# Performance work log

Hardware: AMD Instinct MI355X
Metric: run time of the kernel (lower is better)

Reference implementation:

```python
import jax, jax.numpy as jnp
import numpy as np

B, GRID, DM, DEPTH = 4, 12, 384, 8
L = GRID ** 3                      # 1728 tokens
DI, NS, DC, DTR = 768, 16, 4, 24   # d_inner, d_state, d_conv, dt_rank
KEEP = 432


def _sincos_pos_embed(grid, dim):
    g = np.arange(grid, dtype=np.float32)
    gh, gw, gd = np.meshgrid(g, g, g, indexing='ij')
    pd = dim // 6
    omega = 1.0 / (10000.0 ** (np.arange(pd, dtype=np.float32) / pd))
    parts = []
    for v in (gh, gw, gd):
        o = np.einsum('m,d->md', v.reshape(-1), omega)
        parts += [np.sin(o), np.cos(o)]
    return np.concatenate(parts, axis=1)[None].astype(np.float32)  # (1, L, dim)


def setup_inputs():
    key = jax.random.key(0)
    ks = jax.random.split(key, 16)
    n = lambda k, s, sc=0.02: jax.random.normal(k, s, jnp.float32) * sc
    # mamba dt_proj bias init: inverse softplus of dt ~ LogUniform(1e-3, 1e-1)
    dt = jnp.exp(jax.random.uniform(ks[9], (DEPTH, DI)) * (np.log(0.1) - np.log(0.001)) + np.log(0.001))
    dt_proj_b = dt + jnp.log(-jnp.expm1(-dt))
    A_log = jnp.log(jnp.broadcast_to(jnp.arange(1, NS + 1, dtype=jnp.float32), (DEPTH, DI, NS)))
    rng = np.random.default_rng(0)
    act = np.zeros((B, L), np.int32)
    for b in range(B):
        act[b, rng.permutation(L)[:KEEP]] = 1
    return {
        'imgs': n(ks[0], (B, DM, GRID, GRID, GRID), 1.0),
        'pos_embed': jnp.asarray(_sincos_pos_embed(GRID, DM)),
        'mask_token': n(ks[1], (DM,)),
        'norm1_w': jnp.ones((DEPTH, DM)), 'norm1_b': jnp.zeros((DEPTH, DM)),
        'in_proj_w': n(ks[2], (DEPTH, 2 * DI, DM)),
        'conv_w': n(ks[3], (DEPTH, DI, DC), 0.1), 'conv_b': jnp.zeros((DEPTH, DI)),
        'x_proj_w': n(ks[4], (DEPTH, DTR + 2 * NS, DI)),
        'dt_proj_w': n(ks[5], (DEPTH, DI, DTR), 0.1), 'dt_proj_b': dt_proj_b,
        'A_log': A_log, 'A_b_log': A_log,
        'D_skip': jnp.ones((DEPTH, DI)),
        'out_proj_w': n(ks[6], (DEPTH, DM, DI)),
        'norm2_w': jnp.ones((DEPTH, DM)), 'norm2_b': jnp.zeros((DEPTH, DM)),
        'fc1_w': n(ks[7], (DEPTH, 2 * DM, DM)), 'fc1_b': jnp.zeros((DEPTH, 2 * DM)),
        'fc2_w': n(ks[8], (DEPTH, DM, 2 * DM)), 'fc2_b': jnp.zeros((DEPTH, DM)),
        'active': jnp.asarray(act.reshape(B, 1, GRID, GRID, GRID)),
        'len_keep': KEEP,
    }


def _ln(x, w, b):
    mu = jnp.mean(x, -1, keepdims=True)
    v = jnp.var(x, -1, keepdims=True)
    return (x - mu) * jax.lax.rsqrt(v + 1e-5) * w + b


def _ssm_dir(xr, z, conv_w, conv_b, xpw, dtw, dtb, a_log, dskip):
    # xr, z: (B, DI, Lk) pre-conv streams; causal depthwise conv then selective scan
    Lk = xr.shape[-1]
    xp = jnp.pad(xr, ((0, 0), (0, 0), (DC - 1, 0)))
    x = sum(conv_w[:, k][None, :, None] * xp[:, :, k:k + Lk] for k in range(DC))
    x = jax.nn.silu(x + conv_b[None, :, None])
    xdb = jnp.einsum('bdl,rd->brl', x, xpw)
    dtr, Bm, Cm = xdb[:, :DTR], xdb[:, DTR:DTR + NS], xdb[:, DTR + NS:]
    delta = jax.nn.softplus(jnp.einsum('brl,dr->bdl', dtr, dtw) + dtb[None, :, None])
    A = -jnp.exp(a_log)                              # (DI, NS)
    dl = delta.transpose(0, 2, 1)                    # (B, Lk, DI)
    xt = x.transpose(0, 2, 1)                        # (B, Lk, DI)
    dA = jnp.exp(dl[..., None] * A)                  # (B, Lk, DI, NS)
    dBx = dl[..., None] * Bm.transpose(0, 2, 1)[:, :, None, :] * xt[..., None]
    Ct = Cm.transpose(0, 2, 1)                       # (B, Lk, NS)

    def step(h, inp):
        a, bx, c = inp
        h = a * h + bx
        return h, jnp.einsum('bdn,bn->bd', h, c)

    h0 = jnp.zeros((xr.shape[0], DI, NS), xr.dtype)
    _, ys = jax.lax.scan(step, h0, (dA.transpose(1, 0, 2, 3), dBx.transpose(1, 0, 2, 3), Ct.transpose(1, 0, 2)))
    y = ys.transpose(1, 0, 2) + dskip * xt           # (B, Lk, DI)
    return y * jax.nn.silu(z.transpose(0, 2, 1))


def _block(x, p):
    (n1w, n1b, inW, cw, cb, xpw, dtw, dtb, al, abl, dsk, ow, n2w, n2b, f1w, f1b, f2w, f2b) = p
    h = _ln(x, n1w, n1b)
    xz = h @ inW.T                                   # (B, Lk, 2*DI)
    xr = xz[..., :DI].transpose(0, 2, 1)
    z = xz[..., DI:].transpose(0, 2, 1)
    yf = _ssm_dir(xr, z, cw, cb, xpw, dtw, dtb, al, dsk)
    yb = _ssm_dir(xr[:, :, ::-1], z[:, :, ::-1], cw, cb, xpw, dtw, dtb, abl, dsk)[:, ::-1]
    x = x + (yf + yb) @ ow.T
    h2 = _ln(x, n2w, n2b)
    return x + (jax.nn.gelu(h2 @ f1w.T + f1b, approximate=False) @ f2w.T + f2b)


def _forward(imgs, pos_embed, mask_token, norm1_w, norm1_b, in_proj_w, conv_w, conv_b,
             x_proj_w, dt_proj_w, dt_proj_b, A_log, A_b_log, D_skip, out_proj_w,
             norm2_w, norm2_b, fc1_w, fc1_b, fc2_w, fc2_b, active, len_keep):
    x = imgs.reshape(B, DM, L).transpose(0, 2, 1) + pos_embed   # (B, L, DM)
    mask = active.reshape(B, L).astype(jnp.int32)               # (B, L) 1=keep
    ids_shuffle = jnp.argsort(1 - mask, axis=1)                 # kept tokens first
    ids_restore = jnp.argsort(ids_shuffle, axis=1)
    ids_keep = ids_shuffle[:, :len_keep]
    xk = jnp.take_along_axis(x, jnp.broadcast_to(ids_keep[:, :, None], (B, len_keep, DM)), axis=1)
    blk = jax.checkpoint(_block)
    for i in range(DEPTH):
        p = (norm1_w[i], norm1_b[i], in_proj_w[i], conv_w[i], conv_b[i], x_proj_w[i],
             dt_proj_w[i], dt_proj_b[i], A_log[i], A_b_log[i], D_skip[i], out_proj_w[i],
             norm2_w[i], norm2_b[i], fc1_w[i], fc1_b[i], fc2_w[i], fc2_b[i])
        xk = blk(xk, p)
    mt = jnp.broadcast_to(mask_token, (B, L - len_keep, DM))
    x_ = jnp.concatenate([xk, mt], axis=1)
    x = jnp.take_along_axis(x_, jnp.broadcast_to(ids_restore[:, :, None], (B, L, DM)), axis=1)
    return x.transpose(0, 2, 1).reshape(B, DM, GRID, GRID, GRID)


def reference(imgs, pos_embed, mask_token, norm1_w, norm1_b, in_proj_w, conv_w, conv_b,
              x_proj_w, dt_proj_w, dt_proj_b, A_log, A_b_log, D_skip, out_proj_w,
              norm2_w, norm2_b, fc1_w, fc1_b, fc2_w, fc2_b, active, len_keep):
    return _forward(imgs, pos_embed, mask_token, norm1_w, norm1_b, in_proj_w, conv_w, conv_b,
                    x_proj_w, dt_proj_w, dt_proj_b, A_log, A_b_log, D_skip, out_proj_w,
                    norm2_w, norm2_b, fc1_w, fc1_b, fc2_w, fc2_b, active, len_keep)
```

## Files before the change

### kernel.cpp

```cpp
#include <hip/hip_runtime.h>
#include <hip/hip_bf16.h>
#include <math.h>

#define B_    4
#define GRID_ 12
#define DM_   384
#define DEPTH_ 8
#define L_    1728
#define DI_   768
#define NS_   16
#define DC_   4
#define DTR_  24
#define KEEP_ 432
#define XPR_  56
#define NC_   16
#define CL_   27
#define XSPLIT_ 4

typedef __attribute__((ext_vector_type(8))) short short8;
typedef __attribute__((ext_vector_type(4))) float floatx4;

__device__ __forceinline__ float silu_f(float x) {
    return x / (1.0f + __expf(-x));
}
__device__ __forceinline__ float softplus_f(float x) {
    return (x > 20.0f) ? x : log1pf(expf(x));
}
__device__ __forceinline__ float gelu_exact_f(float x) {
    return 0.5f * x * (1.0f + erff(x * 0.7071067811865476f));
}
__device__ __forceinline__ unsigned short f2bf(float x) {
    union { float f; unsigned int u; } c; c.f = x;
    unsigned int u = c.u;
    unsigned int r = (u + 0x7fffu + ((u >> 16) & 1u)) >> 16;
    return (unsigned short)r;
}

#define S0_ (DEPTH_ * 2 * DI_ * DM_)
#define S1_ (DEPTH_ * XPR_ * DI_)
#define S3_ (DEPTH_ * DM_ * DI_)
#define S4_ (DEPTH_ * 2 * DM_ * DM_)
#define S5_ (DEPTH_ * DM_ * 2 * DM_)
#define WTOT_ (S0_ + S1_ + S3_ + S4_ + S5_)

__global__ void cast_weights_k(const float* __restrict__ w0,
                               const float* __restrict__ w1,
                               const float* __restrict__ w3,
                               const float* __restrict__ w4,
                               const float* __restrict__ w5,
                               unsigned short* __restrict__ out) {
    int i = blockIdx.x * 256 + threadIdx.x;
    if (i >= WTOT_) return;
    float v;
    if (i < S0_) v = w0[i];
    else if (i < S0_ + S1_) v = w1[i - S0_];
    else if (i < S0_ + S1_ + S3_) v = w3[i - S0_ - S1_];
    else if (i < S0_ + S1_ + S3_ + S4_) v = w4[i - S0_ - S1_ - S3_];
    else v = w5[i - S0_ - S1_ - S3_ - S4_];
    out[i] = f2bf(v);
}

__global__ __launch_bounds__(256) void compute_ids_k(
        const int* __restrict__ active,
        int* __restrict__ RANK, int* __restrict__ IDS) {
    __shared__ int cnt[256];
    int b = blockIdx.x;
    int t = threadIdx.x;
    const int PER = (L_ + 255) / 256;
    int base = t * PER;
    int c = 0;
    for (int j = 0; j < PER; ++j) {
        int l = base + j;
        if (l < L_ && active[b * L_ + l]) ++c;
    }
    cnt[t] = c;
    __syncthreads();
    for (int off = 1; off < 256; off <<= 1) {
        int v = (t >= off) ? cnt[t - off] : 0;
        __syncthreads();
        cnt[t] += v;
        __syncthreads();
    }
    int r = cnt[t] - c;
    for (int j = 0; j < PER; ++j) {
        int l = base + j;
        if (l >= L_) break;
        if (active[b * L_ + l]) {
            RANK[b * L_ + l] = r;
            IDS[b * KEEP_ + r] = l;
            ++r;
        } else {
            RANK[b * L_ + l] = -1;
        }
    }
}

__global__ void gather_embed_k(const float* __restrict__ imgs,
                               const float* __restrict__ pos,
                               const int* __restrict__ IDS,
                               float* __restrict__ X) {
    int tid = blockIdx.x * 256 + threadIdx.x;
    if (tid >= B_ * KEEP_ * DM_) return;
    int c = tid % DM_;
    int i = (tid / DM_) % KEEP_;
    int b = tid / (DM_ * KEEP_);
    int l = IDS[b * KEEP_ + i];
    X[tid] = imgs[((size_t)b * DM_ + c) * L_ + l] + pos[(size_t)l * DM_ + c];
}

__global__ void final_scatter_k(const float* __restrict__ X,
                                const float* __restrict__ mask_token,
                                const int* __restrict__ RANK,
                                float* __restrict__ out) {
    int tid = blockIdx.x * 256 + threadIdx.x;
    if (tid >= B_ * DM_ * L_) return;
    int l = tid % L_;
    int c = (tid / L_) % DM_;
    int b = tid / (L_ * DM_);
    int r = RANK[b * L_ + l];
    out[tid] = (r >= 0) ? X[((size_t)b * KEEP_ + r) * DM_ + c] : mask_token[c];
}

__global__ void layernorm_k(const float* __restrict__ X,
                            const float* __restrict__ w,
                            const float* __restrict__ bia,
                            unsigned short* __restrict__ H, int rows) {
    int row = blockIdx.x * 4 + (threadIdx.x >> 6);
    int lane = threadIdx.x & 63;
    if (row >= rows) return;
    const float* x = X + (size_t)row * DM_;
    float v[6];
    float s = 0.0f;
#pragma unroll
    for (int j = 0; j < 6; ++j) { v[j] = x[lane + 64 * j]; s += v[j]; }
#pragma unroll
    for (int m = 1; m < 64; m <<= 1) s += __shfl_xor(s, m);
    float mu = s * (1.0f / DM_);
    float s2 = 0.0f;
#pragma unroll
    for (int j = 0; j < 6; ++j) { float d = v[j] - mu; s2 += d * d; }
#pragma unroll
    for (int m = 1; m < 64; m <<= 1) s2 += __shfl_xor(s2, m);
    float rs = rsqrtf(s2 * (1.0f / DM_) + 1e-5f);
    unsigned short* h = H + (size_t)row * DM_;
#pragma unroll
    for (int j = 0; j < 6; ++j) {
        int c = lane + 64 * j;
        h[c] = f2bf((v[j] - mu) * rs * w[c] + bia[c]);
    }
}

#define APAD_ 40
__global__ __launch_bounds__(256) void gemm_mfma_k(
    const void* __restrict__ Ap, const float* __restrict__ A2, int lda,
    int abf16,
    const unsigned short* __restrict__ Wb,
    const float* __restrict__ bias,
    float* __restrict__ C, int ldc,
    int M, int N, int K, int kslices, int mode) {
    __shared__ unsigned short As[2][64][APAD_];
    __shared__ unsigned short Bs[2][64][APAD_];
    int t = threadIdx.x;
    int wave = t >> 6;
    int lane = t & 63;
    int q = lane >> 4;
    int ml = lane & 15;
    int m0 = blockIdx.y * 64;
    int n0 = blockIdx.x * 64;
    int z  = blockIdx.z;
    int Kper = K / kslices;
    int kbeg = z * Kper;

    int srow = t >> 2;
    int scol = (t & 3) * 8;

    floatx4 acc[4];
#pragma unroll
    for (int i = 0; i < 4; ++i) acc[i] = (floatx4){0.f, 0.f, 0.f, 0.f};

    float ra[8];
    uint4 rau, rb;

    auto loadA = [&](int k0) {
        if (abf16) {
            rau = *(const uint4*)((const unsigned short*)Ap +
                                  (size_t)(m0 + srow) * lda + k0 + scol);
        } else {
            const float* ap = (const float*)Ap + (size_t)(m0 + srow) * lda + k0 + scol;
            floatx4 v0 = *(const floatx4*)ap;
            floatx4 v1 = *(const floatx4*)(ap + 4);
            if (A2) {
                const float* ap2 = A2 + (size_t)(m0 + srow) * lda + k0 + scol;
                v0 += *(const floatx4*)ap2;
                v1 += *(const floatx4*)(ap2 + 4);
            }
#pragma unroll
            for (int j = 0; j < 4; ++j) { ra[j] = v0[j]; ra[4 + j] = v1[j]; }
        }
    };
    auto loadB = [&](int k0) {
        rb = *(const uint4*)(Wb + (size_t)(n0 + srow) * K + k0 + scol);
    };
    auto storeT = [&](int buf) {
        if (abf16) {
            *(uint4*)&As[buf][srow][scol] = rau;
        } else {
#pragma unroll
            for (int j = 0; j < 8; ++j) As[buf][srow][scol + j] = f2bf(ra[j]);
        }
        *(uint4*)&Bs[buf][srow][scol] = rb;
    };

    int nk = Kper >> 5;
    loadA(kbeg);
    loadB(kbeg);
    storeT(0);
    __syncthreads();
    int buf = 0;
    for (int it = 0; it < nk; ++it) {
        if (it + 1 < nk) {
            int kn = kbeg + (it + 1) * 32;
            loadA(kn);
            loadB(kn);
        }
        short8 a = *(const short8*)&As[buf][wave * 16 + ml][q * 8];
#pragma unroll
        for (int ns = 0; ns < 4; ++ns) {
            short8 b = *(const short8*)&Bs[buf][ns * 16 + ml][q * 8];
            acc[ns] = __builtin_amdgcn_mfma_f32_16x16x32_bf16(a, b, acc[ns], 0, 0, 0);
        }
        if (it + 1 < nk) {
            storeT(buf ^ 1);
            __syncthreads();
            buf ^= 1;
        }
    }

#pragma unroll
    for (int ns = 0; ns < 4; ++ns) {
        int n = n0 + ns * 16 + ml;
#pragma unroll
        for (int r = 0; r < 4; ++r) {
            int m = m0 + wave * 16 + q * 4 + r;
            float v = acc[ns][r];
            size_t ci = (size_t)m * ldc + n;
            if (mode == 6) {
                atomicAdd(&C[ci], v);
            } else if (mode == 7) {
                if (z == 0) v += bias[n];
                atomicAdd(&C[ci], v);
            } else if (mode == 9) {
                ((unsigned short*)C)[ci] = f2bf(gelu_exact_f(v + bias[n]));
            } else {
                C[ci] = v;
            }
        }
    }
}

__global__ __launch_bounds__(256) void xproj_conv_k(
        const float* __restrict__ XZ,
        const float* __restrict__ cw,
        const float* __restrict__ cb,
        const unsigned short* __restrict__ Wb,
        float* __restrict__ Cout) {
    __shared__ unsigned short As[2][64][APAD_];
    __shared__ unsigned short Bs[2][64][APAD_];
    int t = threadIdx.x;
    int wave = t >> 6;
    int lane = t & 63;
    int q = lane >> 4;
    int ml = lane & 15;
    int m0 = blockIdx.y * 64;
    int z  = blockIdx.z;
    const int Kper = DI_ / XSPLIT_;
    int kbeg = z * Kper;
    float* C = Cout + (size_t)z * (2 * B_ * KEEP_) * XPR_;

    int srow = t >> 2;
    int scol = (t & 3) * 8;
    int m = m0 + srow;
    int dir = m / (B_ * KEEP_);
    int rem = m - dir * (B_ * KEEP_);
    int b = rem / KEEP_;
    int s = rem - b * KEEP_;

    floatx4 acc[4];
#pragma unroll
    for (int i = 0; i < 4; ++i) acc[i] = (floatx4){0.f, 0.f, 0.f, 0.f};

    float ra[8];
    uint4 rb;

    auto loadA = [&](int k0) {
        int d0 = k0 + scol;
        float v[8];
        {
            floatx4 c0v = *(const floatx4*)(cb + d0);
            floatx4 c1v = *(const floatx4*)(cb + d0 + 4);
#pragma unroll
            for (int j = 0; j < 4; ++j) { v[j] = c0v[j]; v[4 + j] = c1v[j]; }
        }
        float cwv[8][4];
#pragma unroll
        for (int jj = 0; jj < 8; ++jj) {
            floatx4 cv = *(const floatx4*)(cw + (size_t)(d0 + jj) * 4);
#pragma unroll
            for (int j = 0; j < 4; ++j) cwv[jj][j] = cv[j];
        }
#pragma unroll
        for (int j = 0; j < DC_; ++j) {
            int pos = s - (DC_ - 1) + j;
            if (pos >= 0) {
                int la = dir ? (KEEP_ - 1 - pos) : pos;
                const float* xp = XZ + ((size_t)b * KEEP_ + la) * (2 * DI_) + d0;
                floatx4 x0 = *(const floatx4*)xp;
                floatx4 x1 = *(const floatx4*)(xp + 4);
#pragma unroll
                for (int jj = 0; jj < 4; ++jj) v[jj] += cwv[jj][j] * x0[jj];
#pragma unroll
                for (int jj = 0; jj < 4; ++jj) v[4 + jj] += cwv[4 + jj][j] * x1[jj];
            }
        }
#pragma unroll
        for (int jj = 0; jj < 8; ++jj) ra[jj] = silu_f(v[jj]);
    };
    auto loadB = [&](int k0) {
        if (srow < XPR_) {
            rb = *(const uint4*)(Wb + (size_t)srow * DI_ + k0 + scol);
        } else {
            rb = (uint4){0u, 0u, 0u, 0u};
        }
    };
    auto storeT = [&](int buf) {
#pragma unroll
        for (int j = 0; j < 8; ++j) As[buf][srow][scol + j] = f2bf(ra[j]);
        *(uint4*)&Bs[buf][srow][scol] = rb;
    };

    const int nk = Kper >> 5;
    loadA(kbeg);
    loadB(kbeg);
    storeT(0);
    __syncthreads();
    int buf = 0;
    for (int it = 0; it < nk; ++it) {
        if (it + 1 < nk) {
            int kn = kbeg + (it + 1) * 32;
            loadA(kn);
            loadB(kn);
        }
        short8 a = *(const short8*)&As[buf][wave * 16 + ml][q * 8];
#pragma unroll
        for (int ns = 0; ns < 4; ++ns) {
            short8 b2 = *(const short8*)&Bs[buf][ns * 16 + ml][q * 8];
            acc[ns] = __builtin_amdgcn_mfma_f32_16x16x32_bf16(a, b2, acc[ns], 0, 0, 0);
        }
        if (it + 1 < nk) {
            storeT(buf ^ 1);
            __syncthreads();
            buf ^= 1;
        }
    }
#pragma unroll
    for (int ns = 0; ns < 4; ++ns) {
        int n = ns * 16 + ml;
        if (n >= XPR_) continue;
#pragma unroll
        for (int r = 0; r < 4; ++r) {
            int mm = m0 + wave * 16 + q * 4 + r;
            C[(size_t)mm * XPR_ + n] = acc[ns][r];
        }
    }
}

#define PSL_ ((size_t)(2 * B_ * KEEP_) * XPR_)

__global__ __launch_bounds__(256) void scan_partial_k(
        const float* __restrict__ XZ,
        const float* __restrict__ PART,
        const float* __restrict__ cw,
        const float* __restrict__ cb,
        const float* __restrict__ dtw,
        const float* __restrict__ dtb,
        const float* __restrict__ Alog,
        const float* __restrict__ Ablog,
        float* __restrict__ HFIN,
        float* __restrict__ SDELT) {
    __shared__ float sXR[CL_ + 3][256];
    __shared__ float sXDB[CL_][XPR_];
    int blk = blockIdx.x;
    int g   = blk % 3;
    int c   = (blk / 3) % NC_;
    int b   = (blk / (3 * NC_)) % B_;
    int dir = blk / (3 * NC_ * B_);
    int t = threadIdx.x;
    int d = g * 256 + t;
    int c0 = c * CL_;

    for (int r = 0; r < CL_ + 3; ++r) {
        int pos = c0 - 3 + r;
        float v = 0.0f;
        if (pos >= 0) {
            int la = dir ? (KEEP_ - 1 - pos) : pos;
            v = XZ[((size_t)b * KEEP_ + la) * (2 * DI_) + d];
        }
        sXR[r][t] = v;
    }
    size_t rbase = ((size_t)(dir * B_ + b) * KEEP_ + c0) * XPR_;
    for (int i = t; i < CL_ * XPR_; i += 256) {
        size_t idx = rbase + i;
        float v = PART[idx];
#pragma unroll
        for (int sl = 1; sl < XSPLIT_; ++sl) v += PART[idx + sl * PSL_];
        sXDB[i / XPR_][i % XPR_] = v;
    }
    __syncthreads();

    float cwv[DC_];
    {
        floatx4 cv = *(const floatx4*)(cw + (size_t)d * 4);
#pragma unroll
        for (int j = 0; j < DC_; ++j) cwv[j] = cv[j];
    }
    float cbv = cb[d];
    float dtwv[DTR_];
#pragma unroll
    for (int r = 0; r < DTR_ / 4; ++r) {
        floatx4 v = *(const floatx4*)(dtw + (size_t)d * DTR_ + r * 4);
#pragma unroll
        for (int j = 0; j < 4; ++j) dtwv[r * 4 + j] = v[j];
    }
    float dtbv = dtb[d];
    const float* alog = dir ? Ablog : Alog;
    float Av[NS_];
#pragma unroll
    for (int n = 0; n < NS_; ++n) Av[n] = -__expf(alog[(size_t)d * NS_ + n]);

    float h[NS_];
#pragma unroll
    for (int n = 0; n < NS_; ++n) h[n] = 0.0f;
    float sdel = 0.0f;

    for (int s = 0; s < CL_; ++s) {
        float xv = cbv;
#pragma unroll
        for (int j = 0; j < DC_; ++j) xv += cwv[j] * sXR[s + j][t];
        xv = silu_f(xv);
        float dt = dtbv;
#pragma unroll
        for (int r = 0; r < DTR_; ++r) dt += dtwv[r] * sXDB[s][r];
        dt = softplus_f(dt);
        sdel += dt;
        float dx = dt * xv;
#pragma unroll
        for (int n = 0; n < NS_; ++n)
            h[n] = __expf(dt * Av[n]) * h[n] + dx * sXDB[s][DTR_ + n];
    }
    size_t o = ((size_t)(dir * B_ + b) * NC_ + c) * DI_ + d;
    SDELT[o] = sdel;
#pragma unroll
    for (int n = 0; n < NS_; ++n) HFIN[o * NS_ + n] = h[n];
}

__global__ __launch_bounds__(256) void scan_combine_k(
        const float* __restrict__ HFIN,
        const float* __restrict__ SDELT,
        const float* __restrict__ Alog,
        const float* __restrict__ Ablog,
        float* __restrict__ HINIT) {
    int gid = blockIdx.x * 256 + threadIdx.x;
    int n = gid & 15;
    int d = (gid >> 4) % DI_;
    int b = (gid / (16 * DI_)) % B_;
    int dir = gid / (16 * DI_ * B_);
    const float* alog = dir ? Ablog : Alog;
    float Av = -__expf(alog[(size_t)d * NS_ + n]);
    float hi = 0.0f;
#pragma unroll
    for (int c = 0; c < NC_; ++c) {
        size_t o = ((size_t)(dir * B_ + b) * NC_ + c) * DI_ + d;
        HINIT[o * NS_ + n] = hi;
        hi = __expf(Av * SDELT[o]) * hi + HFIN[o * NS_ + n];
    }
}

__global__ __launch_bounds__(256) void scan_final_k(
        const float* __restrict__ XZ,
        const float* __restrict__ PART,
        const float* __restrict__ cw,
        const float* __restrict__ cb,
        const float* __restrict__ dtw,
        const float* __restrict__ dtb,
        const float* __restrict__ Alog,
        const float* __restrict__ Ablog,
        const float* __restrict__ dskip,
        const float* __restrict__ HINIT,
        float* __restrict__ YOUT) {
    __shared__ float sXR[CL_ + 3][256];
    __shared__ float sZ[CL_][256];
    __shared__ float sXDB[CL_][XPR_];
    int blk = blockIdx.x;
    int g   = blk % 3;
    int c   = (blk / 3) % NC_;
    int b   = (blk / (3 * NC_)) % B_;
    int dir = blk / (3 * NC_ * B_);
    int t = threadIdx.x;
    int d = g * 256 + t;
    int c0 = c * CL_;

    for (int r = 0; r < CL_ + 3; ++r) {
        int pos = c0 - 3 + r;
        float v = 0.0f;
        if (pos >= 0) {
            int la = dir ? (KEEP_ - 1 - pos) : pos;
            v = XZ[((size_t)b * KEEP_ + la) * (2 * DI_) + d];
        }
        sXR[r][t] = v;
    }
    for (int s = 0; s < CL_; ++s) {
        int pos = c0 + s;
        int la = dir ? (KEEP_ - 1 - pos) : pos;
        sZ[s][t] = XZ[((size_t)b * KEEP_ + la) * (2 * DI_) + DI_ + d];
    }
    size_t rbase = ((size_t)(dir * B_ + b) * KEEP_ + c0) * XPR_;
    for (int i = t; i < CL_ * XPR_; i += 256) {
        size_t idx = rbase + i;
        float v = PART[idx];
#pragma unroll
        for (int sl = 1; sl < XSPLIT_; ++sl) v += PART[idx + sl * PSL_];
        sXDB[i / XPR_][i % XPR_] = v;
    }
    __syncthreads();

    float cwv[DC_];
    {
        floatx4 cv = *(const floatx4*)(cw + (size_t)d * 4);
#pragma unroll
        for (int j = 0; j < DC_; ++j) cwv[j] = cv[j];
    }
    float cbv = cb[d];
    float dtwv[DTR_];
#pragma unroll
    for (int r = 0; r < DTR_ / 4; ++r) {
        floatx4 v = *(const floatx4*)(dtw + (size_t)d * DTR_ + r * 4);
#pragma unroll
        for (int j = 0; j < 4; ++j) dtwv[r * 4 + j] = v[j];
    }
    float dtbv = dtb[d];
    const float* alog = dir ? Ablog : Alog;
    float Av[NS_];
#pragma unroll
    for (int n = 0; n < NS_; ++n) Av[n] = -__expf(alog[(size_t)d * NS_ + n]);
    float dsk = dskip[d];

    size_t o = ((size_t)(dir * B_ + b) * NC_ + c) * DI_ + d;
    float h[NS_];
#pragma unroll
    for (int n = 0; n < NS_; ++n) h[n] = HINIT[o * NS_ + n];

    for (int s = 0; s < CL_; ++s) {
        float xv = cbv;
#pragma unroll
        for (int j = 0; j < DC_; ++j) xv += cwv[j] * sXR[s + j][t];
        xv = silu_f(xv);
        float dt = dtbv;
#pragma unroll
        for (int r = 0; r < DTR_; ++r) dt += dtwv[r] * sXDB[s][r];
        dt = softplus_f(dt);
        float dx = dt * xv;
        float y = 0.0f;
#pragma unroll
        for (int n = 0; n < NS_; ++n) {
            h[n] = __expf(dt * Av[n]) * h[n] + dx * sXDB[s][DTR_ + n];
            y += h[n] * sXDB[s][DTR_ + NS_ + n];
        }
        int pos = c0 + s;
        int la = dir ? (KEEP_ - 1 - pos) : pos;
        YOUT[((size_t)(dir * B_ + b) * KEEP_ + la) * DI_ + d] =
            (y + dsk * xv) * silu_f(sZ[s][t]);
    }
}

extern "C" void kernel_launch(void* const* d_in, const int* in_sizes, int n_in,
                              void* d_out, int out_size, void* d_ws, size_t ws_size,
                              hipStream_t stream) {
    const float* imgs      = (const float*)d_in[0];
    const float* pos       = (const float*)d_in[1];
    const float* mask_tok  = (const float*)d_in[2];
    const float* n1w       = (const float*)d_in[3];
    const float* n1b       = (const float*)d_in[4];
    const float* inW       = (const float*)d_in[5];
    const float* cw        = (const float*)d_in[6];
    const float* cb        = (const float*)d_in[7];
    const float* xpw       = (const float*)d_in[8];
    const float* dtw       = (const float*)d_in[9];
    const float* dtb       = (const float*)d_in[10];
    const float* Alog      = (const float*)d_in[11];
    const float* Ablog     = (const float*)d_in[12];
    const float* dskip     = (const float*)d_in[13];
    const float* ow        = (const float*)d_in[14];
    const float* n2w       = (const float*)d_in[15];
    const float* n2b       = (const float*)d_in[16];
    const float* f1w       = (const float*)d_in[17];
    const float* f1b       = (const float*)d_in[18];
    const float* f2w       = (const float*)d_in[19];
    const float* f2b       = (const float*)d_in[20];
    const int*   active    = (const int*)d_in[21];
    float* out = (float*)d_out;

    char* w = (char*)d_ws;
    auto alloc = [&](size_t bytes) {
        void* p = (void*)w;
        w += (bytes + 255) & ~(size_t)255;
        return p;
    };
    int*   RANK  = (int*)  alloc((size_t)B_ * L_ * 4);
    int*   IDS   = (int*)  alloc((size_t)B_ * KEEP_ * 4);
    float* X     = (float*)alloc((size_t)B_ * KEEP_ * DM_ * 4);
    unsigned short* Hb = (unsigned short*)alloc((size_t)B_ * KEEP_ * DM_ * 2);
    float* XZ    = (float*)alloc((size_t)B_ * KEEP_ * 2 * DI_ * 4);
    float* PART  = (float*)alloc((size_t)XSPLIT_ * 2 * B_ * KEEP_ * XPR_ * 4);
    float* YOUT  = (float*)alloc((size_t)2 * B_ * KEEP_ * DI_ * 4);
    unsigned short* Gb = (unsigned short*)alloc((size_t)B_ * KEEP_ * DI_ * 2);
    float* HFIN  = (float*)alloc((size_t)2 * B_ * NC_ * DI_ * NS_ * 4);
    float* HINIT = (float*)alloc((size_t)2 * B_ * NC_ * DI_ * NS_ * 4);
    float* SDELT = (float*)alloc((size_t)2 * B_ * NC_ * DI_ * 4);
    unsigned short* WB = (unsigned short*)alloc((size_t)WTOT_ * 2);

    const unsigned short* wInB = WB;
    const unsigned short* wXpB = WB + S0_;
    const unsigned short* wOwB = WB + S0_ + S1_;
    const unsigned short* wF1B = WB + S0_ + S1_ + S3_;
    const unsigned short* wF2B = WB + S0_ + S1_ + S3_ + S4_;

    const int ROWS = B_ * KEEP_;
    const int ROWS2 = 2 * B_ * KEEP_;
    const int SCAN_BLOCKS = 2 * B_ * NC_ * 3;

    cast_weights_k<<<(WTOT_ + 255) / 256, 256, 0, stream>>>(
        inW, xpw, ow, f1w, f2w, (unsigned short*)WB);
    compute_ids_k<<<B_, 256, 0, stream>>>(active, RANK, IDS);
    gather_embed_k<<<(B_ * KEEP_ * DM_ + 255) / 256, 256, 0, stream>>>(imgs, pos, IDS, X);

    for (int layer = 0; layer < DEPTH_; ++layer) {
        const unsigned short* L_inW = wInB + (size_t)layer * 2 * DI_ * DM_;
        const float* L_cw  = cw  + (size_t)layer * DI_ * DC_;
        const float* L_cb  = cb  + (size_t)layer * DI_;
        const unsigned short* L_xpw = wXpB + (size_t)layer * XPR_ * DI_;
        const float* L_dtw = dtw + (size_t)layer * DI_ * DTR_;
        const float* L_dtb = dtb + (size_t)layer * DI_;
        const float* L_Al  = Alog  + (size_t)layer * DI_ * NS_;
        const float* L_Abl = Ablog + (size_t)layer * DI_ * NS_;
        const float* L_dsk = dskip + (size_t)layer * DI_;
        const unsigned short* L_ow  = wOwB + (size_t)layer * DM_ * DI_;
        const unsigned short* L_f1w = wF1B + (size_t)layer * 2 * DM_ * DM_;
        const float* L_f1b = f1b + (size_t)layer * 2 * DM_;
        const unsigned short* L_f2w = wF2B + (size_t)layer * DM_ * 2 * DM_;
        const float* L_f2b = f2b + (size_t)layer * DM_;

        layernorm_k<<<(ROWS + 3) / 4, 256, 0, stream>>>(
            X, n1w + layer * DM_, n1b + layer * DM_, Hb, ROWS);
        gemm_mfma_k<<<dim3((2 * DI_) / 64, ROWS / 64), 256, 0, stream>>>(
            Hb, nullptr, DM_, 1, L_inW, nullptr, XZ, 2 * DI_,
            ROWS, 2 * DI_, DM_, 1, 0);
        xproj_conv_k<<<dim3(1, ROWS2 / 64, XSPLIT_), 256, 0, stream>>>(
            XZ, L_cw, L_cb, L_xpw, PART);
        scan_partial_k<<<SCAN_BLOCKS, 256, 0, stream>>>(
            XZ, PART, L_cw, L_cb, L_dtw, L_dtb, L_Al, L_Abl, HFIN, SDELT);
        scan_combine_k<<<(2 * B_ * DI_ * NS_) / 256, 256, 0, stream>>>(
            HFIN, SDELT, L_Al, L_Abl, HINIT);
        scan_final_k<<<SCAN_BLOCKS, 256, 0, stream>>>(
            XZ, PART, L_cw, L_cb, L_dtw, L_dtb, L_Al, L_Abl, L_dsk, HINIT, YOUT);
        gemm_mfma_k<<<dim3(DM_ / 64, ROWS / 64, 2), 256, 0, stream>>>(
            YOUT, YOUT + (size_t)B_ * KEEP_ * DI_, DI_, 0, L_ow, nullptr,
            X, DM_, ROWS, DM_, DI_, 2, 6);
        layernorm_k<<<(ROWS + 3) / 4, 256, 0, stream>>>(
            X, n2w + layer * DM_, n2b + layer * DM_, Hb, ROWS);
        gemm_mfma_k<<<dim3((2 * DM_) / 64, ROWS / 64), 256, 0, stream>>>(
            Hb, nullptr, DM_, 1, L_f1w, L_f1b, (float*)Gb, 2 * DM_,
            ROWS, 2 * DM_, DM_, 1, 9);
        gemm_mfma_k<<<dim3(DM_ / 64, ROWS / 64, 2), 256, 0, stream>>>(
            Gb, nullptr, 2 * DM_, 1, L_f2w, L_f2b, X, DM_,
            ROWS, DM_, 2 * DM_, 2, 7);
    }

    final_scatter_k<<<(B_ * DM_ * L_ + 255) / 256, 256, 0, stream>>>(
        X, mask_tok, RANK, out);
}
```

Before: 1.488 ms.

## Exploit geometric A structure in scan, shorten chunks, drop shared staging

Scan kernels check at runtime whether A_n equals (n+1)*A_0 and, if so, compute the per-state decays as successive powers of one exponential instead of 16 exps. Chunk length drops from 27 to 9 (48 chunks) to raise parallelism, conv inputs are streamed through registers instead of shared memory, and softplus uses fast intrinsics. The chunk-state buffers are merged into one d-contiguous array updated in place by the combine kernel. It risks a longer serial combine and slight precision differences from the power chaining.

```diff
diff --git a/kernel.cpp b/kernel.cpp
--- a/kernel.cpp
+++ b/kernel.cpp
@@ -13,8 +13,8 @@
 #define DTR_  24
 #define KEEP_ 432
 #define XPR_  56
-#define NC_   16
-#define CL_   27
+#define NC_   48
+#define CL_   9
 #define XSPLIT_ 4
 
 typedef __attribute__((ext_vector_type(8))) short short8;
@@ -24,7 +24,7 @@
     return x / (1.0f + __expf(-x));
 }
 __device__ __forceinline__ float softplus_f(float x) {
-    return (x > 20.0f) ? x : log1pf(expf(x));
+    return (x > 20.0f) ? x : __logf(1.0f + __expf(x));
 }
 __device__ __forceinline__ float gelu_exact_f(float x) {
     return 0.5f * x * (1.0f + erff(x * 0.7071067811865476f));
@@ -376,6 +376,18 @@
 
 #define PSL_ ((size_t)(2 * B_ * KEEP_) * XPR_)
 
+__device__ __forceinline__ bool a_geometric(const float* alog, int d, float& Av0) {
+    Av0 = -__expf(alog[(size_t)d * NS_]);
+    bool fast = true;
+#pragma unroll
+    for (int n = 1; n < NS_; ++n) {
+        float av = -__expf(alog[(size_t)d * NS_ + n]);
+        float ref = (float)(n + 1) * Av0;
+        fast = fast && (fabsf(av - ref) <= 1e-4f * fabsf(ref));
+    }
+    return fast;
+}
+
 __global__ __launch_bounds__(256) void scan_partial_k(
         const float* __restrict__ XZ,
         const float* __restrict__ PART,
@@ -385,9 +397,8 @@
         const float* __restrict__ dtb,
         const float* __restrict__ Alog,
         const float* __restrict__ Ablog,
-        float* __restrict__ HFIN,
+        float* __restrict__ HS,
         float* __restrict__ SDELT) {
-    __shared__ float sXR[CL_ + 3][256];
     __shared__ float sXDB[CL_][XPR_];
     int blk = blockIdx.x;
     int g   = blk % 3;
@@ -397,17 +408,9 @@
     int t = threadIdx.x;
     int d = g * 256 + t;
     int c0 = c * CL_;
-
-    for (int r = 0; r < CL_ + 3; ++r) {
-        int pos = c0 - 3 + r;
-        float v = 0.0f;
-        if (pos >= 0) {
-            int la = dir ? (KEEP_ - 1 - pos) : pos;
-            v = XZ[((size_t)b * KEEP_ + la) * (2 * DI_) + d];
-        }
-        sXR[r][t] = v;
-    }
-    size_t rbase = ((size_t)(dir * B_ + b) * KEEP_ + c0) * XPR_;
+    int dirb = dir * B_ + b;
+
+    size_t rbase = ((size_t)dirb * KEEP_ + c0) * XPR_;
     for (int i = t; i < CL_ * XPR_; i += 256) {
         size_t idx = rbase + i;
         float v = PART[idx];
@@ -417,12 +420,7 @@
     }
     __syncthreads();
 
-    float cwv[DC_];
-    {
-        floatx4 cv = *(const floatx4*)(cw + (size_t)d * 4);
-#pragma unroll
-        for (int j = 0; j < DC_; ++j) cwv[j] = cv[j];
-    }
+    floatx4 cwv = *(const floatx4*)(cw + (size_t)d * 4);
     float cbv = cb[d];
     float dtwv[DTR_];
 #pragma unroll
@@ -433,55 +431,89 @@
     }
     float dtbv = dtb[d];
     const float* alog = dir ? Ablog : Alog;
-    float Av[NS_];
-#pragma unroll
-    for (int n = 0; n < NS_; ++n) Av[n] = -__expf(alog[(size_t)d * NS_ + n]);
+    float Av0;
+    bool fast = a_geometric(alog, d, Av0);
+
+    auto xr_at = [&](int pos) -> float {
+        if (pos < 0) return 0.0f;
+        int la = dir ? (KEEP_ - 1 - pos) : pos;
+        return XZ[((size_t)b * KEEP_ + la) * (2 * DI_) + d];
+    };
+    float w0 = xr_at(c0 - 3), w1 = xr_at(c0 - 2), w2 = xr_at(c0 - 1);
 
     float h[NS_];
 #pragma unroll
     for (int n = 0; n < NS_; ++n) h[n] = 0.0f;
     float sdel = 0.0f;
 
-    for (int s = 0; s < CL_; ++s) {
-        float xv = cbv;
-#pragma unroll
-        for (int j = 0; j < DC_; ++j) xv += cwv[j] * sXR[s + j][t];
-        xv = silu_f(xv);
-        float dt = dtbv;
-#pragma unroll
-        for (int r = 0; r < DTR_; ++r) dt += dtwv[r] * sXDB[s][r];
-        dt = softplus_f(dt);
-        sdel += dt;
-        float dx = dt * xv;
-#pragma unroll
-        for (int n = 0; n < NS_; ++n)
-            h[n] = __expf(dt * Av[n]) * h[n] + dx * sXDB[s][DTR_ + n];
-    }
-    size_t o = ((size_t)(dir * B_ + b) * NC_ + c) * DI_ + d;
-    SDELT[o] = sdel;
-#pragma unroll
-    for (int n = 0; n < NS_; ++n) HFIN[o * NS_ + n] = h[n];
+    if (fast) {
+#pragma unroll
+        for (int s = 0; s < CL_; ++s) {
+            float w3 = xr_at(c0 + s);
+            float xv = silu_f(cbv + cwv[0] * w0 + cwv[1] * w1 + cwv[2] * w2 + cwv[3] * w3);
+            w0 = w1; w1 = w2; w2 = w3;
+            float dt = dtbv;
+#pragma unroll
+            for (int r = 0; r < DTR_; ++r) dt += dtwv[r] * sXDB[s][r];
+            dt = softplus_f(dt);
+            sdel += dt;
+            float dx = dt * xv;
+            float e1 = __expf(dt * Av0);
+            float e = e1;
+#pragma unroll
+            for (int n = 0; n < NS_; ++n) {
+                h[n] = e * h[n] + dx * sXDB[s][DTR_ + n];
+                e *= e1;
+            }
+        }
+    } else {
+        for (int s = 0; s < CL_; ++s) {
+            float w3 = xr_at(c0 + s);
+            float xv = silu_f(cbv + cwv[0] * w0 + cwv[1] * w1 + cwv[2] * w2 + cwv[3] * w3);
+            w0 = w1; w1 = w2; w2 = w3;
+            float dt = dtbv;
+            for (int r = 0; r < DTR_; ++r) dt += dtwv[r] * sXDB[s][r];
+            dt = softplus_f(dt);
+            sdel += dt;
+            float dx = dt * xv;
+            for (int n = 0; n < NS_; ++n) {
+                float av = -__expf(alog[(size_t)d * NS_ + n]);
+                h[n] = __expf(dt * av) * h[n] + dx * sXDB[s][DTR_ + n];
+            }
+        }
+    }
+    size_t ob = ((size_t)dirb * NC_ + c) * NS_;
+    SDELT[((size_t)dirb * NC_ + c) * DI_ + d] = sdel;
+#pragma unroll
+    for (int n = 0; n < NS_; ++n) HS[(ob + n) * DI_ + d] = h[n];
 }
 
 __global__ __launch_bounds__(256) void scan_combine_k(
-        const float* __restrict__ HFIN,
+        float* __restrict__ HS,
         const float* __restrict__ SDELT,
         const float* __restrict__ Alog,
-        const float* __restrict__ Ablog,
-        float* __restrict__ HINIT) {
+        const float* __restrict__ Ablog) {
     int gid = blockIdx.x * 256 + threadIdx.x;
-    int n = gid & 15;
-    int d = (gid >> 4) % DI_;
-    int b = (gid / (16 * DI_)) % B_;
-    int dir = gid / (16 * DI_ * B_);
+    int d = gid % DI_;
+    int n = (gid / DI_) % NS_;
+    int b = (gid / (DI_ * NS_)) % B_;
+    int dir = gid / (DI_ * NS_ * B_);
+    int dirb = dir * B_ + b;
     const float* alog = dir ? Ablog : Alog;
     float Av = -__expf(alog[(size_t)d * NS_ + n]);
     float hi = 0.0f;
-#pragma unroll
+    size_t sbase = (size_t)dirb * NC_ * DI_ + d;
+    size_t hbase = ((size_t)dirb * NC_ * NS_ + n) * DI_ + d;
+    float sd_n = SDELT[sbase];
+    float hf_n = HS[hbase];
     for (int c = 0; c < NC_; ++c) {
-        size_t o = ((size_t)(dir * B_ + b) * NC_ + c) * DI_ + d;
-        HINIT[o * NS_ + n] = hi;
-        hi = __expf(Av * SDELT[o]) * hi + HFIN[o * NS_ + n];
+        float sd = sd_n, hf = hf_n;
+        if (c + 1 < NC_) {
+            sd_n = SDELT[sbase + (size_t)(c + 1) * DI_];
+            hf_n = HS[hbase + (size_t)(c + 1) * NS_ * DI_];
+        }
+        HS[hbase + (size_t)c * NS_ * DI_] = hi;
+        hi = __expf(Av * sd) * hi + hf;
     }
 }
 
@@ -495,10 +527,8 @@
         const float* __restrict__ Alog,
         const float* __restrict__ Ablog,
         const float* __restrict__ dskip,
-        const float* __restrict__ HINIT,
+        const float* __restrict__ HS,
         float* __restrict__ YOUT) {
-    __shared__ float sXR[CL_ + 3][256];
-    __shared__ float sZ[CL_][256];
     __shared__ float sXDB[CL_][XPR_];
     int blk = blockIdx.x;
     int g   = blk % 3;
@@ -508,22 +538,9 @@
     int t = threadIdx.x;
     int d = g * 256 + t;
     int c0 = c * CL_;
-
-    for (int r = 0; r < CL_ + 3; ++r) {
-        int pos = c0 - 3 + r;
-        float v = 0.0f;
-        if (pos >= 0) {
-            int la = dir ? (KEEP_ - 1 - pos) : pos;
-            v = XZ[((size_t)b * KEEP_ + la) * (2 * DI_) + d];
-        }
-        sXR[r][t] = v;
-    }
-    for (int s = 0; s < CL_; ++s) {
-        int pos = c0 + s;
-        int la = dir ? (KEEP_ - 1 - pos) : pos;
-        sZ[s][t] = XZ[((size_t)b * KEEP_ + la) * (2 * DI_) + DI_ + d];
-    }
-    size_t rbase = ((size_t)(dir * B_ + b) * KEEP_ + c0) * XPR_;
+    int dirb = dir * B_ + b;
+
+    size_t rbase = ((size_t)dirb * KEEP_ + c0) * XPR_;
     for (int i = t; i < CL_ * XPR_; i += 256) {
         size_t idx = rbase + i;
         float v = PART[idx];
@@ -533,12 +550,7 @@
     }
     __syncthreads();
 
-    float cwv[DC_];
-    {
-        floatx4 cv = *(const floatx4*)(cw + (size_t)d * 4);
-#pragma unroll
-        for (int j = 0; j < DC_; ++j) cwv[j] = cv[j];
-    }
+    floatx4 cwv = *(const floatx4*)(cw + (size_t)d * 4);
     float cbv = cb[d];
     float dtwv[DTR_];
 #pragma unroll
@@ -549,36 +561,69 @@
     }
     float dtbv = dtb[d];
     const float* alog = dir ? Ablog : Alog;
-    float Av[NS_];
-#pragma unroll
-    for (int n = 0; n < NS_; ++n) Av[n] = -__expf(alog[(size_t)d * NS_ + n]);
+    float Av0;
+    bool fast = a_geometric(alog, d, Av0);
     float dsk = dskip[d];
 
-    size_t o = ((size_t)(dir * B_ + b) * NC_ + c) * DI_ + d;
     float h[NS_];
-#pragma unroll
-    for (int n = 0; n < NS_; ++n) h[n] = HINIT[o * NS_ + n];
-
-    for (int s = 0; s < CL_; ++s) {
-        float xv = cbv;
-#pragma unroll
-        for (int j = 0; j < DC_; ++j) xv += cwv[j] * sXR[s + j][t];
-        xv = silu_f(xv);
-        float dt = dtbv;
-#pragma unroll
-        for (int r = 0; r < DTR_; ++r) dt += dtwv[r] * sXDB[s][r];
-        dt = softplus_f(dt);
-        float dx = dt * xv;
-        float y = 0.0f;
-#pragma unroll
-        for (int n = 0; n < NS_; ++n) {
-            h[n] = __expf(dt * Av[n]) * h[n] + dx * sXDB[s][DTR_ + n];
-            y += h[n] * sXDB[s][DTR_ + NS_ + n];
-        }
-        int pos = c0 + s;
+    size_t hbase = ((size_t)dirb * NC_ + c) * NS_;
+#pragma unroll
+    for (int n = 0; n < NS_; ++n) h[n] = HS[(hbase + n) * DI_ + d];
+
+    auto xr_at = [&](int pos) -> float {
+        if (pos < 0) return 0.0f;
         int la = dir ? (KEEP_ - 1 - pos) : pos;
-        YOUT[((size_t)(dir * B_ + b) * KEEP_ + la) * DI_ + d] =
-            (y + dsk * xv) * silu_f(sZ[s][t]);
+        return XZ[((size_t)b * KEEP_ + la) * (2 * DI_) + d];
+    };
+    float w0 = xr_at(c0 - 3), w1 = xr_at(c0 - 2), w2 = xr_at(c0 - 1);
+
+    if (fast) {
+#pragma unroll
+        for (int s = 0; s < CL_; ++s) {
+            int pos = c0 + s;
+            int la = dir ? (KEEP_ - 1 - pos) : pos;
+            float w3 = XZ[((size_t)b * KEEP_ + la) * (2 * DI_) + d];
+            float zg = XZ[((size_t)b * KEEP_ + la) * (2 * DI_) + DI_ + d];
+            float xv = silu_f(cbv + cwv[0] * w0 + cwv[1] * w1 + cwv[2] * w2 + cwv[3] * w3);
+            w0 = w1; w1 = w2; w2 = w3;
+            float dt = dtbv;
+#pragma unroll
+            for (int r = 0; r < DTR_; ++r) dt += dtwv[r] * sXDB[s][r];
+            dt = softplus_f(dt);
+            float dx = dt * xv;
+            float e1 = __expf(dt * Av0);
+            float e = e1;
+            float y = 0.0f;
+#pragma unroll
+            for (int n = 0; n < NS_; ++n) {
+                h[n] = e * h[n] + dx * sXDB[s][DTR_ + n];
+                y += h[n] * sXDB[s][DTR_ + NS_ + n];
+                e *= e1;
+            }
+            YOUT[((size_t)dirb * KEEP_ + la) * DI_ + d] =
+                (y + dsk * xv) * silu_f(zg);
+        }
+    } else {
+        for (int s = 0; s < CL_; ++s) {
+            int pos = c0 + s;
+            int la = dir ? (KEEP_ - 1 - pos) : pos;
+            float w3 = XZ[((size_t)b * KEEP_ + la) * (2 * DI_) + d];
+            float zg = XZ[((size_t)b * KEEP_ + la) * (2 * DI_) + DI_ + d];
+            float xv = silu_f(cbv + cwv[0] * w0 + cwv[1] * w1 + cwv[2] * w2 + cwv[3] * w3);
+            w0 = w1; w1 = w2; w2 = w3;
+            float dt = dtbv;
+            for (int r = 0; r < DTR_; ++r) dt += dtwv[r] * sXDB[s][r];
+            dt = softplus_f(dt);
+            float dx = dt * xv;
+            float y = 0.0f;
+            for (int n = 0; n < NS_; ++n) {
+                float av = -__expf(alog[(size_t)d * NS_ + n]);
+                h[n] = __expf(dt * av) * h[n] + dx * sXDB[s][DTR_ + n];
+                y += h[n] * sXDB[s][DTR_ + NS_ + n];
+            }
+            YOUT[((size_t)dirb * KEEP_ + la) * DI_ + d] =
+                (y + dsk * xv) * silu_f(zg);
+        }
     }
 }
 
@@ -623,8 +668,7 @@
     float* PART  = (float*)alloc((size_t)XSPLIT_ * 2 * B_ * KEEP_ * XPR_ * 4);
     float* YOUT  = (float*)alloc((size_t)2 * B_ * KEEP_ * DI_ * 4);
     unsigned short* Gb = (unsigned short*)alloc((size_t)B_ * KEEP_ * DI_ * 2);
-    float* HFIN  = (float*)alloc((size_t)2 * B_ * NC_ * DI_ * NS_ * 4);
-    float* HINIT = (float*)alloc((size_t)2 * B_ * NC_ * DI_ * NS_ * 4);
+    float* HS    = (float*)alloc((size_t)2 * B_ * NC_ * NS_ * DI_ * 4);
     float* SDELT = (float*)alloc((size_t)2 * B_ * NC_ * DI_ * 4);
     unsigned short* WB = (unsigned short*)alloc((size_t)WTOT_ * 2);
 
@@ -667,11 +711,11 @@
         xproj_conv_k<<<dim3(1, ROWS2 / 64, XSPLIT_), 256, 0, stream>>>(
             XZ, L_cw, L_cb, L_xpw, PART);
         scan_partial_k<<<SCAN_BLOCKS, 256, 0, stream>>>(
-            XZ, PART, L_cw, L_cb, L_dtw, L_dtb, L_Al, L_Abl, HFIN, SDELT);
-        scan_combine_k<<<(2 * B_ * DI_ * NS_) / 256, 256, 0, stream>>>(
-            HFIN, SDELT, L_Al, L_Abl, HINIT);
+            XZ, PART, L_cw, L_cb, L_dtw, L_dtb, L_Al, L_Abl, HS, SDELT);
+        scan_combine_k<<<(2 * B_ * NS_ * DI_) / 256, 256, 0, stream>>>(
+            HS, SDELT, L_Al, L_Abl);
         scan_final_k<<<SCAN_BLOCKS, 256, 0, stream>>>(
-            XZ, PART, L_cw, L_cb, L_dtw, L_dtb, L_Al, L_Abl, L_dsk, HINIT, YOUT);
+            XZ, PART, L_cw, L_cb, L_dtw, L_dtb, L_Al, L_Abl, L_dsk, HS, YOUT);
         gemm_mfma_k<<<dim3(DM_ / 64, ROWS / 64, 2), 256, 0, stream>>>(
             YOUT, YOUT + (size_t)B_ * KEEP_ * DI_, DI_, 0, L_ow, nullptr,
             X, DM_, ROWS, DM_, DI_, 2, 6);
```

Result: faster. 1.276 ms (-14.3%).
